# Kernel tuning notes

Measured on AMD Instinct MI355X. Metric: run time of the kernel, lower is better.

The kernel has to match this reference:

```python
import jax, jax.numpy as jnp
import numpy as np

B, S, DIM, H = 2, 2048, 2048, 16
NOPE, ROPE, VHD, KLR = 128, 64, 128, 512
QKHD = NOPE + ROPE  # 192
SCALE = QKHD ** -0.5
EPS = 1.1920929e-07  # torch.finfo(float32).eps, nn.RMSNorm default eps


def _rope(x, cos, sin):
    # x: [b, s, h, r]; cos/sin: [s, r//2]; pairs are adjacent elements (view_as_complex convention)
    x2 = x.reshape(*x.shape[:-1], -1, 2)
    xr, xi = x2[..., 0], x2[..., 1]
    c = cos[None, :, None, :]
    s_ = sin[None, :, None, :]
    out = jnp.stack([xr * c - xi * s_, xr * s_ + xi * c], axis=-1)
    return out.reshape(x.shape)


def setup_inputs() -> dict:
    key = jax.random.key(0)
    ks = jax.random.split(key, 5)
    x = jax.random.normal(ks[0], (B, S, DIM), jnp.float32)
    wq = jax.random.normal(ks[1], (H * QKHD, DIM), jnp.float32) * 0.02
    wkv_a = jax.random.normal(ks[2], (KLR + ROPE, DIM), jnp.float32) * 0.02
    kv_norm_w = jnp.ones((KLR,), jnp.float32)
    wkv_b = jax.random.normal(ks[3], (H * (NOPE + VHD), KLR), jnp.float32) * 0.02
    wo = jax.random.normal(ks[4], (DIM, H * VHD), jnp.float32) * 0.02
    # rotary tables (start_pos=0, no YaRN since rope_factor=1 / original_seq_len=None)
    inv_freq = 1.0 / (10000.0 ** (np.arange(0, ROPE, 2, dtype=np.float32) / ROPE))
    ang = np.outer(np.arange(S, dtype=np.float32), inv_freq)
    freqs_cos = jnp.asarray(np.cos(ang))
    freqs_sin = jnp.asarray(np.sin(ang))
    # causal mask [S, S]
    mask = jnp.where(jnp.tril(jnp.ones((S, S), bool)), 0.0, -1e9).astype(jnp.float32)
    return {"x": x, "wq": wq, "wkv_a": wkv_a, "kv_norm_w": kv_norm_w,
            "wkv_b": wkv_b, "wo": wo, "freqs_cos": freqs_cos,
            "freqs_sin": freqs_sin, "mask": mask}


def reference(x, wq, wkv_a, kv_norm_w, wkv_b, wo, freqs_cos, freqs_sin, mask):
    b, s, _ = x.shape
    # query projection (q_lora_rank == 0 path)
    q = (x @ wq.T).reshape(b, s, H, QKHD)
    q_nope, q_pe = q[..., :NOPE], q[..., NOPE:]
    q_pe = _rope(q_pe, freqs_cos, freqs_sin)
    # latent KV projection
    kv = x @ wkv_a.T  # [b, s, KLR + ROPE]
    kv_c, k_pe = kv[..., :KLR], kv[..., KLR:]
    kv_c = kv_c * jax.lax.rsqrt(jnp.mean(kv_c * kv_c, axis=-1, keepdims=True) + EPS) * kv_norm_w
    k_pe = _rope(k_pe[:, :, None, :], freqs_cos, freqs_sin)[:, :, 0]  # [b, s, ROPE]
    # KV-absorption: fold wkv_b's K half into the query
    wb = wkv_b.reshape(H, NOPE + VHD, KLR)
    q_proj = jnp.einsum('bshd,hdc->bshc', q_nope, wb[:, :NOPE])  # [b,s,H,KLR]
    scores = (jnp.einsum('bshc,btc->bsht', q_proj, kv_c)
              + jnp.einsum('bshr,btr->bsht', q_pe, k_pe)) * SCALE
    scores = scores + mask[:, None, :]  # broadcast over heads
    attn = jax.nn.softmax(scores.astype(jnp.float32), axis=-1).astype(x.dtype)
    o = jnp.einsum('bsht,btc->bshc', attn, kv_c)
    o = jnp.einsum('bshc,hdc->bshd', o, wb[:, NOPE:])  # value up-projection
    return o.reshape(b, s, H * VHD) @ wo.T
```

## Files before the change

### kernel.cpp

```cpp
#include <hip/hip_runtime.h>

#define DI __device__ __forceinline__

typedef __bf16 bf16x8 __attribute__((ext_vector_type(8)));
typedef float  f32x4  __attribute__((ext_vector_type(4)));

DI unsigned short f2bf(float f){
  unsigned u = __builtin_bit_cast(unsigned, f);
  u = (u + 0x7fffu + ((u >> 16) & 1u)) >> 16;
  return (unsigned short)u;
}
DI float b2f(unsigned short h){
  return __builtin_bit_cast(float, (unsigned)h << 16);
}
DI f32x4 MFMA(bf16x8 a, bf16x8 b, f32x4 c){
  return __builtin_amdgcn_mfma_f32_16x16x32_bf16(a, b, c, 0, 0, 0);
}
DI void gll16(const void* g, void* l){
  __builtin_amdgcn_global_load_lds((const __attribute__((address_space(1))) void*)g,
                                   (__attribute__((address_space(3))) void*)l,
                                   16, 0, 0);
}


__global__ void k_f2b(const float* __restrict__ in, unsigned short* __restrict__ out, long n){
  long i = ((long)blockIdx.x*256 + threadIdx.x)*4;
  if (i >= n) return;
  float4 v = *(const float4*)(in + i);
  ushort4 r; r.x=f2bf(v.x); r.y=f2bf(v.y); r.z=f2bf(v.z); r.w=f2bf(v.w);
  *(ushort4*)(out + i) = r;
}

__global__ void k_wkva(const float* __restrict__ in, unsigned short* __restrict__ out){
  int idx = blockIdx.x*256 + threadIdx.x;
  long i = (long)idx*4;
  int row = (int)(i >> 11), col = (int)(i & 2047);
  ushort4 r;
  if (row < 576){
    float4 v = *(const float4*)(in + (long)row*2048 + col);
    r.x=f2bf(v.x); r.y=f2bf(v.y); r.z=f2bf(v.z); r.w=f2bf(v.w);
  } else { r.x=0; r.y=0; r.z=0; r.w=0; }
  *(ushort4*)(out + i) = r;
}

__global__ void k_wbkT(const float* __restrict__ wkvb, unsigned short* __restrict__ out){
  int i = blockIdx.x*256 + threadIdx.x;
  int d = i & 127, c = (i>>7)&511, h = i>>16;
  out[i] = f2bf(wkvb[(long)((h<<8) + d)*512 + c]);
}

__global__ void k_ropeq(const unsigned short* __restrict__ q, const float* __restrict__ fc,
                        const float* __restrict__ fs, unsigned short* __restrict__ qkcat){
  int i = blockIdx.x*256 + threadIdx.x;
  int p = i & 31, h = (i>>5)&15, m = i>>9;
  int s = m & 2047;
  const unsigned short* qp = q + (long)m*3072 + h*192 + 128 + (p<<1);
  float xr = b2f(qp[0]), xi = b2f(qp[1]);
  float c = fc[(s<<5)+p], sn = fs[(s<<5)+p];
  unsigned short* dst = qkcat + ((long)m*16 + h)*576 + 512 + (p<<1);
  dst[0] = f2bf(xr*c - xi*sn);
  dst[1] = f2bf(xr*sn + xi*c);
}

__global__ void k_ropek(const unsigned short* __restrict__ kv, const float* __restrict__ fc,
                        const float* __restrict__ fs, unsigned short* __restrict__ kvcat){
  int i = blockIdx.x*256 + threadIdx.x;
  int p = i & 31, m = i>>5;
  int s = m & 2047;
  const unsigned short* kp = kv + (long)m*640 + 512 + (p<<1);
  float xr = b2f(kp[0]), xi = b2f(kp[1]);
  float c = fc[(s<<5)+p], sn = fs[(s<<5)+p];
  unsigned short* dst = kvcat + (long)m*576 + 512 + (p<<1);
  dst[0] = f2bf(xr*c - xi*sn);
  dst[1] = f2bf(xr*sn + xi*c);
}

__global__ __launch_bounds__(256)
void k_kvnorm(const unsigned short* __restrict__ kv, const float* __restrict__ w,
              unsigned short* __restrict__ kvcat){
  int m = blockIdx.x*4 + (threadIdx.x>>6);
  int l = threadIdx.x & 63;
  const unsigned short* row = kv + (long)m*640 + (l<<3);
  float v[8]; float ss = 0.f;
  #pragma unroll
  for (int j=0;j<8;j++){ v[j] = b2f(row[j]); ss += v[j]*v[j]; }
  #pragma unroll
  for (int d=1; d<64; d<<=1) ss += __shfl_xor(ss, d, 64);
  float r = rsqrtf(ss*(1.f/512.f) + 1.1920929e-07f);
  unsigned short* dst = kvcat + (long)m*576 + (l<<3);
  const float* wp = w + (l<<3);
  #pragma unroll
  for (int j=0;j<8;j++) dst[j] = f2bf(v[j]*r*wp[j]);
}

__global__ void k_vt(const unsigned short* __restrict__ kvcat, unsigned short* __restrict__ vt){
  int i = blockIdx.x*256 + threadIdx.x;
  int t = i & 2047, c = (i>>11)&511, b = i>>20;
  vt[i] = kvcat[(long)((b<<11)+t)*576 + c];
}

template<int BF16OUT>
__global__ __launch_bounds__(256, 2)
void gemm_bt(const unsigned short* __restrict__ A, const unsigned short* __restrict__ B,
             void* __restrict__ Cv, int K, int lda, int ldb, int ldc,
             long bsA, long bsB, long bsC)
{
  const int bz = blockIdx.z;
  A += (long)bz*bsA; B += (long)bz*bsB;
  const int m0 = blockIdx.x<<7, n0 = blockIdx.y<<7;
  __shared__ __align__(16) unsigned short lA[128*32];
  __shared__ __align__(16) unsigned short lB[128*32];
  const int tid = threadIdx.x, l = tid&63, w = tid>>6;
  const int li = l&15, g = l>>4;
  const int wm = (w>>1)<<6, wn = (w&1)<<6;
  const int r0 = (l>>2), ce = (l&3)<<3;
  f32x4 acc[4][4];
  #pragma unroll
  for (int a_=0;a_<4;a_++)
    #pragma unroll
    for (int b_=0;b_<4;b_++) acc[a_][b_] = f32x4{0.f,0.f,0.f,0.f};

  for (int k0 = 0; k0 < K; k0 += 32){
    __syncthreads();
    #pragma unroll
    for (int i=0;i<2;i++){
      const int ch = (i<<2) + w;
      const int r  = (ch<<4) + r0;
      gll16(A + (long)(m0+r)*lda + k0 + ce, (char*)lA + (ch<<10));
      gll16(B + (long)(n0+r)*ldb + k0 + ce, (char*)lB + (ch<<10));
    }
    __syncthreads();
    bf16x8 af[4], bfv[4];
    #pragma unroll
    for (int mf=0;mf<4;mf++)
      af[mf] = *(const bf16x8*)((const char*)lA + (wm + (mf<<4) + li)*64 + (g<<4));
    #pragma unroll
    for (int nf=0;nf<4;nf++)
      bfv[nf] = *(const bf16x8*)((const char*)lB + (wn + (nf<<4) + li)*64 + (g<<4));
    #pragma unroll
    for (int mf=0;mf<4;mf++)
      #pragma unroll
      for (int nf=0;nf<4;nf++)
        acc[mf][nf] = MFMA(af[mf], bfv[nf], acc[mf][nf]);
  }
  #pragma unroll
  for (int mf=0;mf<4;mf++)
    #pragma unroll
    for (int nf=0;nf<4;nf++)
      #pragma unroll
      for (int j=0;j<4;j++){
        const int row = m0 + wm + (mf<<4) + (g<<2) + j;
        const int col = n0 + wn + (nf<<4) + li;
        if (BF16OUT)
          ((unsigned short*)Cv)[(long)bz*bsC + (long)row*ldc + col] = f2bf(acc[mf][nf][j]);
        else
          ((float*)Cv)[(long)bz*bsC + (long)row*ldc + col] = acc[mf][nf][j];
      }
}

#define SCALE_F 0.07216878364870322f

__global__ __launch_bounds__(512, 2)
void attn(const unsigned short* __restrict__ qk,
          const unsigned short* __restrict__ kvc,
          const unsigned short* __restrict__ vt,
          unsigned short* __restrict__ o)
{
  const int pi = blockIdx.x, hp = blockIdx.y, b = blockIdx.z;
  const int tid = threadIdx.x, l = tid & 63, w = tid >> 6;
  const int li = l & 15, g = l >> 4;
  const int h  = (hp << 1) + (w >> 2);
  const int rg = w & 3;

  __shared__ __align__(16) unsigned short Kl[2][32*576];
  __shared__ __align__(16) unsigned short Vl[2][512*32];
  __shared__ __align__(16) unsigned short Pl[8][16*40];
  unsigned short* Pw = &Pl[w][0];

  int soff[9];
  const unsigned short* sbase;
  if (w < 4){
    sbase = kvc + (long)(b << 11) * 576;
    #pragma unroll
    for (int i = 0; i < 9; i++){
      int ch = i*256 + tid;
      int r  = ch / 72;
      int cb = (ch - r*72) << 4;
      int cbs = cb ^ ((r & 7) << 4);
      soff[i] = r*576 + (cbs >> 1);
    }
  } else {
    sbase = vt + (long)(b << 9) * 2048;
    #pragma unroll
    for (int i = 0; i < 8; i++){
      int ch = i*256 + (tid - 256);
      int c  = ch >> 2;
      int tb = (ch & 3) << 4;
      int tbs = tb ^ ((c & 3) << 4);
      soff[i] = c*2048 + (tbs >> 1);
    }
    soff[8] = 0;
  }

  auto STAGE = [&](int buf, int kt){
    const int t0 = kt << 5;
    if (w < 4){
      const unsigned short* s = sbase + (long)t0 * 576;
      char* d = (char*)&Kl[buf][0] + tid*16;
      #pragma unroll
      for (int i = 0; i < 9; i++) gll16(s + soff[i], d + i*4096);
    } else {
      const unsigned short* s = sbase + t0;
      char* d = (char*)&Vl[buf][0] + (tid - 256)*16;
      #pragma unroll
      for (int i = 0; i < 8; i++) gll16(s + soff[i], d + i*4096);
    }
  };

  #pragma unroll 1
  for (int half = 0; half < 2; half++){
    const int qt = half ? (31 - pi) : pi;
    const int q0 = (qt << 6) + (rg << 4);
    const int nsteps = (qt << 1) + 2;

    bf16x8 qf[18];
    {
      const unsigned short* qp = qk + ((long)((b<<11) + q0 + li)*16 + h)*576 + (g<<3);
      #pragma unroll
      for (int ks = 0; ks < 18; ks++) qf[ks] = *(const bf16x8*)(qp + ks*32);
    }
    asm volatile("s_waitcnt vmcnt(0)" ::: "memory");
    __builtin_amdgcn_sched_barrier(0);

    f32x4 accO[32];
    #pragma unroll
    for (int i = 0; i < 32; i++) accO[i] = f32x4{0.f,0.f,0.f,0.f};
    float mrow[4] = {-1e30f,-1e30f,-1e30f,-1e30f};
    float lsum[4] = {0.f,0.f,0.f,0.f};

    STAGE(0, 0);
    int cur = 0;

    #pragma unroll 1
    for (int kt = 0; kt < nsteps; kt++){
      const int tn = (kt + 1 < nsteps) ? kt + 1 : kt;
      STAGE(cur ^ 1, tn);
      if (w < 4) asm volatile("s_waitcnt vmcnt(9)" ::: "memory");
      else       asm volatile("s_waitcnt vmcnt(8)" ::: "memory");
      __builtin_amdgcn_sched_barrier(0);
      __builtin_amdgcn_s_barrier();

      const int t0 = kt << 5;
      const char* Kb = (const char*)&Kl[cur][0];
      const char* Vb = (const char*)&Vl[cur][0];
      f32x4 sc0 = f32x4{0.f,0.f,0.f,0.f}, sc1 = f32x4{0.f,0.f,0.f,0.f};
      const int swz = (li & 7) << 4;
      __builtin_amdgcn_s_setprio(1);
      #pragma unroll
      for (int ks = 0; ks < 18; ks++){
        const int cb = ((ks<<6) + (g<<4)) ^ swz;
        bf16x8 k0 = *(const bf16x8*)(Kb + li*1152 + cb);
        bf16x8 k1 = *(const bf16x8*)(Kb + (16+li)*1152 + cb);
        sc0 = MFMA(qf[ks], k0, sc0);
        sc1 = MFMA(qf[ks], k1, sc1);
      }
      __builtin_amdgcn_s_setprio(0);

      float s0v[4], s1v[4];
      #pragma unroll
      for (int j = 0; j < 4; j++){
        const int q = q0 + (g<<2) + j;
        s0v[j] = sc0[j]*SCALE_F;
        s1v[j] = sc1[j]*SCALE_F;
        if (t0 + li      > q) s0v[j] = -1e30f;
        if (t0 + 16 + li > q) s1v[j] = -1e30f;
      }
      bool viol = false;
      #pragma unroll
      for (int j = 0; j < 4; j++)
        viol = viol || (fmaxf(s0v[j], s1v[j]) > mrow[j] + 8.0f);
      if (__any(viol)){
        float cr[4];
        #pragma unroll
        for (int j = 0; j < 4; j++){
          float mx = fmaxf(s0v[j], s1v[j]);
          #pragma unroll
          for (int d = 1; d < 16; d <<= 1) mx = fmaxf(mx, __shfl_xor(mx, d, 64));
          const float mnew = fmaxf(mrow[j], mx);
          cr[j] = __expf(mrow[j] - mnew);
          mrow[j] = mnew;
          lsum[j] *= cr[j];
        }
        #pragma unroll
        for (int nf = 0; nf < 32; nf++){
          f32x4 a = accO[nf];
          a[0]*=cr[0]; a[1]*=cr[1]; a[2]*=cr[2]; a[3]*=cr[3];
          accO[nf] = a;
        }
      }
      #pragma unroll
      for (int j = 0; j < 4; j++){
        const float p0 = __expf(s0v[j] - mrow[j]);
        const float p1 = __expf(s1v[j] - mrow[j]);
        lsum[j] += p0 + p1;
        Pw[((g<<2)+j)*40 + li]      = f2bf(p0);
        Pw[((g<<2)+j)*40 + 16 + li] = f2bf(p1);
      }
      asm volatile("s_waitcnt lgkmcnt(0)" ::: "memory");
      __builtin_amdgcn_sched_barrier(0);
      const bf16x8 pa = *(const bf16x8*)((const char*)Pw + li*80 + (g<<4));
      __builtin_amdgcn_s_setprio(1);
      #pragma unroll
      for (int nf = 0; nf < 32; nf++){
        const int c = (nf<<4) + li;
        bf16x8 vb = *(const bf16x8*)(Vb + c*64 + ((g<<4) ^ ((c&3)<<4)));
        accO[nf] = MFMA(pa, vb, accO[nf]);
      }
      __builtin_amdgcn_s_setprio(0);
      __builtin_amdgcn_sched_barrier(0);
      __builtin_amdgcn_s_barrier();
      cur ^= 1;
    }

    #pragma unroll
    for (int j = 0; j < 4; j++){
      float ls = lsum[j];
      #pragma unroll
      for (int d = 1; d < 16; d <<= 1) ls += __shfl_xor(ls, d, 64);
      const float inv = 1.0f/ls;
      const int q = q0 + (g<<2) + j;
      unsigned short* op = o + ((long)((b<<11) + q)*16 + h)*512 + li;
      #pragma unroll
      for (int nf = 0; nf < 32; nf++) op[nf<<4] = f2bf(accO[nf][j]*inv);
    }
  }
}


extern "C" void kernel_launch(void* const* d_in, const int* in_sizes, int n_in,
                              void* d_out, int out_size, void* d_ws, size_t ws_size,
                              hipStream_t stream)
{
  const float* x    = (const float*)d_in[0];
  const float* wq   = (const float*)d_in[1];
  const float* wkva = (const float*)d_in[2];
  const float* kvw  = (const float*)d_in[3];
  const float* wkvb = (const float*)d_in[4];
  const float* wo   = (const float*)d_in[5];
  const float* fc   = (const float*)d_in[6];
  const float* fs   = (const float*)d_in[7];
  float* out = (float*)d_out;

  char* ws = (char*)d_ws;
  auto alloc = [&](size_t bytes)->void*{
    void* p = ws; ws += (bytes + 255) & ~(size_t)255; return p;
  };
  unsigned short* x_bf    = (unsigned short*)alloc( 8388608ull*2);
  unsigned short* wq_bf   = (unsigned short*)alloc( 6291456ull*2);
  unsigned short* wkva_p  = (unsigned short*)alloc( 1310720ull*2);
  unsigned short* wkvb_bf = (unsigned short*)alloc( 2097152ull*2);
  unsigned short* wbkT    = (unsigned short*)alloc( 1048576ull*2);
  unsigned short* wo_bf   = (unsigned short*)alloc( 4194304ull*2);
  unsigned short* q_bf    = (unsigned short*)alloc(12582912ull*2);
  unsigned short* kv_bf   = (unsigned short*)alloc( 2621440ull*2);
  unsigned short* qkcat   = (unsigned short*)alloc(37748736ull*2);
  unsigned short* kvcat   = (unsigned short*)alloc( 2359296ull*2);
  unsigned short* vtb     = (unsigned short*)alloc( 2097152ull*2);
  unsigned short* obuf    = (unsigned short*)alloc(33554432ull*2);
  unsigned short* o2      = (unsigned short*)alloc( 8388608ull*2);

  k_f2b <<<8192,256,0,stream>>>(x,    x_bf,    8388608);
  k_f2b <<<6144,256,0,stream>>>(wq,   wq_bf,   6291456);
  k_wkva<<<1280,256,0,stream>>>(wkva, wkva_p);
  k_f2b <<<2048,256,0,stream>>>(wkvb, wkvb_bf, 2097152);
  k_wbkT<<<4096,256,0,stream>>>(wkvb, wbkT);
  k_f2b <<<4096,256,0,stream>>>(wo,   wo_bf,   4194304);

  gemm_bt<1><<<dim3(32,24,1),256,0,stream>>>(x_bf, wq_bf, q_bf, 2048, 2048, 2048, 3072, 0,0,0);
  gemm_bt<1><<<dim3(32,5,1),256,0,stream>>>(x_bf, wkva_p, kv_bf, 2048, 2048, 2048, 640, 0,0,0);

  k_ropeq <<<8192,256,0,stream>>>(q_bf, fc, fs, qkcat);
  k_kvnorm<<<1024,256,0,stream>>>(kv_bf, kvw, kvcat);
  k_ropek <<<512, 256,0,stream>>>(kv_bf, fc, fs, kvcat);

  gemm_bt<1><<<dim3(32,4,16),256,0,stream>>>(q_bf, wbkT, qkcat, 128, 3072, 128, 9216,
                                             192, 65536, 576);
  k_vt<<<8192,256,0,stream>>>(kvcat, vtb);

  attn<<<dim3(16,8,2),512,0,stream>>>(qkcat, kvcat, vtb, obuf);

  gemm_bt<1><<<dim3(32,1,16),256,0,stream>>>(obuf, wkvb_bf + 65536, o2, 512, 8192, 512, 2048,
                                             512, 131072, 128);
  gemm_bt<0><<<dim3(32,16,1),256,0,stream>>>(o2, wo_bf, out, 2048, 2048, 2048, 2048, 0,0,0);
}
```

Baseline: 698.3 us.

## Restructure attention to one head per 256-thread block, single-buffered LDS

```diff
diff --git a/kernel.cpp b/kernel.cpp
--- a/kernel.cpp
+++ b/kernel.cpp
@@ -160,61 +160,53 @@
 
 #define SCALE_F 0.07216878364870322f
 
-__global__ __launch_bounds__(512, 2)
+__global__ __launch_bounds__(256, 2)
 void attn(const unsigned short* __restrict__ qk,
           const unsigned short* __restrict__ kvc,
           const unsigned short* __restrict__ vt,
           unsigned short* __restrict__ o)
 {
-  const int pi = blockIdx.x, hp = blockIdx.y, b = blockIdx.z;
+  const int pi = blockIdx.x, h = blockIdx.y, b = blockIdx.z;
   const int tid = threadIdx.x, l = tid & 63, w = tid >> 6;
   const int li = l & 15, g = l >> 4;
-  const int h  = (hp << 1) + (w >> 2);
-  const int rg = w & 3;
-
-  __shared__ __align__(16) unsigned short Kl[2][32*576];
-  __shared__ __align__(16) unsigned short Vl[2][512*32];
-  __shared__ __align__(16) unsigned short Pl[8][16*40];
+  const int rg = w;
+
+  __shared__ __align__(16) unsigned short Kl[32*576];
+  __shared__ __align__(16) unsigned short Vl[256*64];
+  __shared__ __align__(16) unsigned short Pl[4][16*40];
   unsigned short* Pw = &Pl[w][0];
 
-  int soff[9];
-  const unsigned short* sbase;
-  if (w < 4){
-    sbase = kvc + (long)(b << 11) * 576;
-    #pragma unroll
-    for (int i = 0; i < 9; i++){
-      int ch = i*256 + tid;
-      int r  = ch / 72;
-      int cb = (ch - r*72) << 4;
-      int cbs = cb ^ ((r & 7) << 4);
-      soff[i] = r*576 + (cbs >> 1);
-    }
-  } else {
-    sbase = vt + (long)(b << 9) * 2048;
-    #pragma unroll
-    for (int i = 0; i < 8; i++){
-      int ch = i*256 + (tid - 256);
-      int c  = ch >> 2;
-      int tb = (ch & 3) << 4;
-      int tbs = tb ^ ((c & 3) << 4);
-      soff[i] = c*2048 + (tbs >> 1);
-    }
-    soff[8] = 0;
+  int soff_k[9];
+  #pragma unroll
+  for (int i = 0; i < 9; i++){
+    int ch = i*256 + tid;
+    int r  = ch / 72;
+    int c  = ch - r*72;
+    int cs = c ^ (r & 7);
+    soff_k[i] = r*576 + (cs << 3);
   }
-
-  auto STAGE = [&](int buf, int kt){
+  int soff_v[8];
+  #pragma unroll
+  for (int i = 0; i < 8; i++){
+    int ch = i*256 + tid;
+    int r  = ch >> 3;
+    int chk = (ch & 7) ^ (r & 7);
+    int c  = (r << 1) + (chk >> 2);
+    soff_v[i] = c*2048 + ((chk & 3) << 3);
+  }
+  const unsigned short* sbase = kvc + (long)(b << 11)*576;
+  const unsigned short* vbase = vt  + (long)(b << 9)*2048;
+
+  auto STAGE = [&](int kt){
     const int t0 = kt << 5;
-    if (w < 4){
-      const unsigned short* s = sbase + (long)t0 * 576;
-      char* d = (char*)&Kl[buf][0] + tid*16;
-      #pragma unroll
-      for (int i = 0; i < 9; i++) gll16(s + soff[i], d + i*4096);
-    } else {
-      const unsigned short* s = sbase + t0;
-      char* d = (char*)&Vl[buf][0] + (tid - 256)*16;
-      #pragma unroll
-      for (int i = 0; i < 8; i++) gll16(s + soff[i], d + i*4096);
-    }
+    const unsigned short* sk = sbase + (long)t0*576;
+    char* dk = (char*)Kl + tid*16;
+    #pragma unroll
+    for (int i = 0; i < 9; i++) gll16(sk + soff_k[i], dk + i*4096);
+    const unsigned short* sv = vbase + t0;
+    char* dv = (char*)Vl + tid*16;
+    #pragma unroll
+    for (int i = 0; i < 8; i++) gll16(sv + soff_v[i], dv + i*4096);
   };
 
   #pragma unroll 1
@@ -229,8 +221,6 @@
       #pragma unroll
       for (int ks = 0; ks < 18; ks++) qf[ks] = *(const bf16x8*)(qp + ks*32);
     }
-    asm volatile("s_waitcnt vmcnt(0)" ::: "memory");
-    __builtin_amdgcn_sched_barrier(0);
 
     f32x4 accO[32];
     #pragma unroll
@@ -238,21 +228,16 @@
     float mrow[4] = {-1e30f,-1e30f,-1e30f,-1e30f};
     float lsum[4] = {0.f,0.f,0.f,0.f};
 
-    STAGE(0, 0);
-    int cur = 0;
-
     #pragma unroll 1
     for (int kt = 0; kt < nsteps; kt++){
-      const int tn = (kt + 1 < nsteps) ? kt + 1 : kt;
-      STAGE(cur ^ 1, tn);
-      if (w < 4) asm volatile("s_waitcnt vmcnt(9)" ::: "memory");
-      else       asm volatile("s_waitcnt vmcnt(8)" ::: "memory");
+      STAGE(kt);
+      asm volatile("s_waitcnt vmcnt(0)" ::: "memory");
       __builtin_amdgcn_sched_barrier(0);
       __builtin_amdgcn_s_barrier();
 
       const int t0 = kt << 5;
-      const char* Kb = (const char*)&Kl[cur][0];
-      const char* Vb = (const char*)&Vl[cur][0];
+      const char* Kb = (const char*)Kl;
+      const char* Vb = (const char*)Vl;
       f32x4 sc0 = f32x4{0.f,0.f,0.f,0.f}, sc1 = f32x4{0.f,0.f,0.f,0.f};
       const int swz = (li & 7) << 4;
       __builtin_amdgcn_s_setprio(1);
@@ -313,13 +298,13 @@
       #pragma unroll
       for (int nf = 0; nf < 32; nf++){
         const int c = (nf<<4) + li;
-        bf16x8 vb = *(const bf16x8*)(Vb + c*64 + ((g<<4) ^ ((c&3)<<4)));
+        const int chk = (((c&1)<<2) + g) ^ ((c>>1)&7);
+        bf16x8 vb = *(const bf16x8*)(Vb + (c>>1)*128 + chk*16);
         accO[nf] = MFMA(pa, vb, accO[nf]);
       }
       __builtin_amdgcn_s_setprio(0);
       __builtin_amdgcn_sched_barrier(0);
       __builtin_amdgcn_s_barrier();
-      cur ^= 1;
     }
 
     #pragma unroll
@@ -387,7 +372,7 @@
                                              192, 65536, 576);
   k_vt<<<8192,256,0,stream>>>(kvcat, vtb);
 
-  attn<<<dim3(16,8,2),512,0,stream>>>(qkcat, kvcat, vtb, obuf);
+  attn<<<dim3(16,16,2),256,0,stream>>>(qkcat, kvcat, vtb, obuf);
 
   gemm_bt<1><<<dim3(32,1,16),256,0,stream>>>(obuf, wkvb_bf + 65536, o2, 512, 8192, 512, 2048,
                                              512, 131072, 128);
```

Measured after the change: 812.6 us. 16.4% more time.
